# Kernel tuning notes

Measured on AMD Instinct MI355X. Metric: run time of the kernel, lower is better.

Reference implementation:

```python
import jax, jax.numpy as jnp
import numpy as np

B, T, H, HEADS, OUT = 16, 8192, 256, 2, 5
PERIOD = 16  # phoneme boundary every 16 frames
EPS_DENOM = 1e-5
LN_EPS = 1e-5
TEMP = 1.0


def setup_inputs() -> dict:
    key = jax.random.key(0)
    ks = jax.random.split(key, 8)
    s = 0.02
    feat = jax.random.normal(ks[0], (B, T, H), jnp.float32)
    ph_bd = jnp.broadcast_to(((jnp.arange(T) % PERIOD) == PERIOD - 1).astype(jnp.int32), (B, T))
    ph_length = T // PERIOD + 1  # 513
    return {
        'feat': feat,
        'ph_bd': ph_bd,
        'ph_length': ph_length,
        'w_attn': jax.random.normal(ks[1], (HEADS, H), jnp.float32) * s,
        'b_attn': jnp.zeros((HEADS,), jnp.float32),
        'ln1_g': jnp.ones((H,), jnp.float32),
        'ln1_b': jnp.zeros((H,), jnp.float32),
        'conv1_w': jax.random.normal(ks[2], (H, H, 3), jnp.float32) * s,
        'conv1_b': jnp.zeros((H,), jnp.float32),
        'conv2_w': jax.random.normal(ks[3], (H, H, 1), jnp.float32) * s,
        'conv2_b': jnp.zeros((H,), jnp.float32),
        'ln2_g': jnp.ones((H,), jnp.float32),
        'ln2_b': jnp.zeros((H,), jnp.float32),
        'post_w': jax.random.normal(ks[4], (H, H, 3), jnp.float32) * s,
        'post_b': jnp.zeros((H,), jnp.float32),
        'w_out': jax.random.normal(ks[5], (OUT, H), jnp.float32) * s,
        'b_out': jnp.zeros((OUT,), jnp.float32),
    }


def _ln_c(x, g, b):
    # LayerNorm over channel dim of [B, C, L]
    m = jnp.mean(x, axis=1, keepdims=True)
    v = jnp.mean((x - m) ** 2, axis=1, keepdims=True)
    return (x - m) * jax.lax.rsqrt(v + LN_EPS) * g[None, :, None] + b[None, :, None]


def _conv1d(x, w, b):
    # x: [B, C, L], w: [O, I, K], 'same' padding
    pad = (w.shape[-1] - 1) // 2
    y = jax.lax.conv_general_dilated(x, w, (1,), [(pad, pad)],
                                     dimension_numbers=('NCH', 'OIH', 'NCH'))
    return y + b[None, :, None]


def reference(feat, ph_bd, ph_length, w_attn, b_attn, ln1_g, ln1_b,
              conv1_w, conv1_b, conv2_w, conv2_b, ln2_g, ln2_b,
              post_w, post_b, w_out, b_out):
    # multihead attention weights per frame: [B, T, heads]
    attn = jax.nn.sigmoid(jnp.einsum('bth,ah->bta', feat, w_attn) + b_attn)
    attn_mean = jnp.mean(attn, axis=-1)                 # [B, T]
    # mean over heads of feat[...,None]*attn == feat * mean(attn)
    attn_feat = feat * attn_mean[..., None]             # [B, T, H]

    mel2ph = jnp.cumsum(ph_bd, axis=1)                  # [B, T] frame->phoneme id
    bidx = jnp.arange(feat.shape[0])[:, None]
    denom = jnp.zeros((feat.shape[0], ph_length), feat.dtype).at[bidx, mel2ph].add(attn_mean)
    ph_agg = jnp.zeros((feat.shape[0], ph_length, feat.shape[2]), feat.dtype).at[bidx, mel2ph].add(attn_feat)
    ph_agg = ph_agg / (denom[..., None] + EPS_DENOM)    # [B, L, H]

    # ConvBlocks (1 residual block, layers_in_block=1, c_multiple=1, swish)
    x = jnp.transpose(ph_agg, (0, 2, 1))                # [B, H, L]
    nonpad = (jnp.sum(jnp.abs(x), axis=1) > 0).astype(x.dtype)[:, None, :]
    h = _ln_c(x, ln1_g, ln1_b)
    h = _conv1d(h, conv1_w, conv1_b) * (3.0 ** -0.5)
    h = jax.nn.silu(h)
    h = _conv1d(h, conv2_w, conv2_b)
    x = (x + h) * nonpad
    x = _ln_c(x, ln2_g, ln2_b) * nonpad
    x = _conv1d(x, post_w, post_b) * nonpad
    out = jnp.transpose(x, (0, 2, 1))                   # [B, L, H]

    tech_logits = (jnp.einsum('blh,oh->blo', out, w_out) + b_out) / TEMP
    return tech_logits
```

## Files before the change

### kernel.cpp

```cpp
#include <hip/hip_runtime.h>
#include <hip/hip_bf16.h>

#define TDIM 8192
#define BDIM 16
#define HDIM 256
#define PHL  513
#define PADL 515
#define MROWS (BDIM*PHL)
#define SEGW 514

typedef __attribute__((ext_vector_type(8))) short  short8;
typedef __attribute__((ext_vector_type(4))) float  floatx4;

__device__ __forceinline__ float sigmoidf_(float x){ return 1.0f/(1.0f+__expf(-x)); }

typedef __attribute__((address_space(1))) const unsigned int gu32;
typedef __attribute__((address_space(3))) unsigned int lu32;
__device__ __forceinline__ void g2l16(const void* g, void* l){
  __builtin_amdgcn_global_load_lds((gu32*)g, (lu32*)l, 16, 0, 0);
}

__device__ __forceinline__ float blk_reduce(float v, float* red){
  #pragma unroll
  for (int off=32; off>0; off>>=1) v += __shfl_xor(v, off, 64);
  int w = threadIdx.x>>6;
  __syncthreads();
  if ((threadIdx.x&63)==0) red[w]=v;
  __syncthreads();
  return red[0]+red[1]+red[2]+red[3];
}

__global__ __launch_bounds__(256) void k_scan(const int* __restrict__ ph_bd,
                                              int* __restrict__ seg){
  int b = blockIdx.x, tid = threadIdx.x;
  const int* in = ph_bd + (size_t)b*TDIM;
  int sb = b*SEGW;
  int base = tid*32;
  int vals[32]; int s=0;
  #pragma unroll
  for (int i=0;i<32;i+=4){
    int4 v = *(const int4*)(in+base+i);
    vals[i]=v.x; vals[i+1]=v.y; vals[i+2]=v.z; vals[i+3]=v.w;
    s += v.x+v.y+v.z+v.w;
  }
  __shared__ int ls[256];
  ls[tid]=s; __syncthreads();
  for (int off=1; off<256; off<<=1){
    int t = (tid>=off)? ls[tid-off] : 0;
    __syncthreads();
    ls[tid]+=t;
    __syncthreads();
  }
  int cur = ls[tid]-s;
  #pragma unroll
  for (int i=0;i<32;i++){
    int nxt = cur + vals[i];
    for (int v=cur+1; v<=nxt; v++) seg[sb+v] = base+i;
    cur = nxt;
  }
  if (tid==0) seg[sb] = 0;
  if (tid==255){ for (int v=cur+1; v<SEGW; v++) seg[sb+v] = TDIM; }
}

__global__ __launch_bounds__(256) void k_prep(
    const float* __restrict__ conv1_w, const float* __restrict__ conv2_w,
    const float* __restrict__ post_w,
    __bf16* __restrict__ w1t, __bf16* __restrict__ w2t, __bf16* __restrict__ w3t,
    int* __restrict__ rowoff,
    float* __restrict__ x0pad, __bf16* __restrict__ h1pad, __bf16* __restrict__ x2pad)
{
  int idx = blockIdx.x*256 + threadIdx.x;
  if (idx < 256*768){
    int o = idx/768, j = idx - o*768;
    int dl = j>>8, i = j&255;
    int src = (o*256+i)*3 + dl;
    w1t[idx] = (__bf16)conv1_w[src];
    w3t[idx] = (__bf16)post_w[src];
  }
  if (idx < 256*256)
    w2t[idx] = (__bf16)conv2_w[idx];
  if (idx < MROWS){
    int b = idx/513, l = idx - b*513;
    rowoff[idx] = (b*PADL + l)*HDIM;
  }
  if (idx < BDIM*2*HDIM){
    int b = idx>>9, rr=(idx>>8)&1, c=idx&255;
    size_t row = (size_t)b*PADL + (rr? (PADL-1):0);
    x0pad[row*HDIM+c]=0.f;
    h1pad[row*HDIM+c]=(__bf16)0.f;
    x2pad[row*HDIM+c]=(__bf16)0.f;
  }
}

__global__ __launch_bounds__(256) void k_attn(
    const float* __restrict__ feat, const int* __restrict__ seg,
    const float* __restrict__ w_attn, const float* __restrict__ b_attn,
    const float* __restrict__ ln1_g, const float* __restrict__ ln1_b,
    float* __restrict__ x0pad, __bf16* __restrict__ h1pad, float* __restrict__ nonpad)
{
  int b = blockIdx.x / PHL, p = blockIdx.x - b*PHL;
  int tid = threadIdx.x, lane = tid&63, w = tid>>6;
  __shared__ float4 sfeat[16*64];
  __shared__ float sam[16];
  __shared__ float red[4];

  int t0 = seg[b*SEGW + p], t1 = seg[b*SEGW + p + 1];

  float4 wa0 = ((const float4*)w_attn)[lane];
  float4 wa1 = ((const float4*)(w_attn+HDIM))[lane];
  float ba0 = b_attn[0], ba1 = b_attn[1];

  float agg=0.f, denom=0.f;
  for (int base=t0; base<t1; base+=16){
    int nf = min(16, t1-base);
    const float4* src = (const float4*)(feat + ((size_t)b*TDIM + base)*HDIM);
    for (int idx=tid; idx<nf*64; idx+=256) sfeat[idx] = src[idx];
    __syncthreads();
    for (int ft=w; ft<nf; ft+=4){
      float4 f = sfeat[ft*64+lane];
      float d0 = f.x*wa0.x + f.y*wa0.y + f.z*wa0.z + f.w*wa0.w;
      float d1 = f.x*wa1.x + f.y*wa1.y + f.z*wa1.z + f.w*wa1.w;
      #pragma unroll
      for (int off=32;off>0;off>>=1){ d0+=__shfl_xor(d0,off,64); d1+=__shfl_xor(d1,off,64); }
      if (lane==0) sam[ft] = 0.5f*(sigmoidf_(d0+ba0)+sigmoidf_(d1+ba1));
    }
    __syncthreads();
    const float* sf = (const float*)sfeat;
    for (int ft=0; ft<nf; ft++){ float a=sam[ft]; agg += sf[ft*HDIM+tid]*a; denom += a; }
    __syncthreads();
  }

  float x = agg/(denom+1e-5f);
  float sabs = blk_reduce(fabsf(x), red);
  float np = (sabs>0.f)?1.f:0.f;
  float mean = blk_reduce(x, red)*(1.f/HDIM);
  float d = x-mean;
  float var = blk_reduce(d*d, red)*(1.f/HDIM);
  float h = d*rsqrtf(var+1e-5f)*ln1_g[tid]+ln1_b[tid];

  size_t off = ((size_t)b*PADL + p + 1)*HDIM;
  x0pad[off+tid]=x;
  h1pad[off+tid]=(__bf16)h;
  if (tid==0) nonpad[blockIdx.x]=np;
}

__global__ __launch_bounds__(256) void k_convblock(
    const short* __restrict__ h1pad, const int* __restrict__ rowoff,
    const short* __restrict__ w1t, const short* __restrict__ w2t,
    const float* __restrict__ c1b, const float* __restrict__ c2b,
    const float* __restrict__ x0pad, const float* __restrict__ nonpad,
    const float* __restrict__ g2, const float* __restrict__ b2,
    __bf16* __restrict__ x2pad)
{
  __shared__ __align__(16) short As[4*64*8];
  __shared__ __align__(16) short Bs[4*256*8];
  __shared__ __align__(16) short Gt[32*64*8];
  int tid=threadIdx.x, lane=tid&63, w=tid>>6, quad=lane>>4, l15=lane&15;
  int m0 = blockIdx.x*64;
  int am = min(m0 + lane, MROWS-1);
  const short* aRow = h1pad + rowoff[am];
  short* AsW = &As[w*64*8];

  floatx4 acc[16];
  #pragma unroll
  for (int i=0;i<16;i++) acc[i] = (floatx4){0.f,0.f,0.f,0.f};

  for (int chunk=0; chunk<24; chunk++){
    int k0 = chunk*32;
    g2l16(aRow + k0 + w*8, AsW);
    #pragma unroll
    for (int ng=0; ng<4; ng++)
      g2l16(w1t + (size_t)(ng*64+lane)*768 + k0 + w*8, &Bs[(w*256 + ng*64)*8]);
    __syncthreads();
    short8 af = *(const short8*)&As[(quad*64 + w*16 + l15)*8];
    #pragma unroll
    for (int nt=0; nt<16; nt++){
      short8 bf = *(const short8*)&Bs[(quad*256 + nt*16 + l15)*8];
      acc[nt] = __builtin_amdgcn_mfma_f32_16x16x32_bf16(af, bf, acc[nt], 0,0,0);
    }
    __syncthreads();
  }

  const float inv_s3 = 0.57735026918962576f;
  #pragma unroll
  for (int nt=0; nt<16; nt++){
    int n = nt*16 + l15;
    float bias = c1b[n];
    #pragma unroll
    for (int r=0;r<4;r++){
      float v = (acc[nt][r] + bias)*inv_s3;
      v = v*sigmoidf_(v);
      int ml = w*16 + quad*4 + r;
      ((__bf16*)Gt)[((n>>3)*64 + ml)*8 + (n&7)] = (__bf16)v;
    }
  }

  floatx4 acc2[16];
  #pragma unroll
  for (int i=0;i<16;i++) acc2[i] = (floatx4){0.f,0.f,0.f,0.f};
  for (int chunk=0; chunk<8; chunk++){
    int k0 = chunk*32;
    #pragma unroll
    for (int ng=0; ng<4; ng++)
      g2l16(w2t + (size_t)(ng*64+lane)*256 + k0 + w*8, &Bs[(w*256 + ng*64)*8]);
    __syncthreads();
    short8 af = *(const short8*)&Gt[((chunk*4+quad)*64 + w*16 + l15)*8];
    #pragma unroll
    for (int nt=0; nt<16; nt++){
      short8 bf = *(const short8*)&Bs[(quad*256 + nt*16 + l15)*8];
      acc2[nt] = __builtin_amdgcn_mfma_f32_16x16x32_bf16(af, bf, acc2[nt], 0,0,0);
    }
    __syncthreads();
  }

  int mbase = m0 + w*16 + quad*4;
  float np_[4]; const float* x0b[4]; int roff[4];
  #pragma unroll
  for (int r=0;r<4;r++){
    int m = min(mbase + r, MROWS-1);
    np_[r] = nonpad[m];
    roff[r] = rowoff[m] + HDIM;
    x0b[r] = x0pad + roff[r];
  }
  float sum[4]={0,0,0,0}, ssq[4]={0,0,0,0};
  #pragma unroll
  for (int nt=0; nt<16; nt++){
    int n = nt*16 + l15;
    float cb = c2b[n];
    #pragma unroll
    for (int r=0;r<4;r++){
      float x = (x0b[r][n] + acc2[nt][r] + cb)*np_[r];
      acc2[nt][r] = x;
      sum[r]+=x; ssq[r]+=x*x;
    }
  }
  #pragma unroll
  for (int off=1; off<16; off<<=1){
    #pragma unroll
    for (int r=0;r<4;r++){ sum[r]+=__shfl_xor(sum[r],off,64); ssq[r]+=__shfl_xor(ssq[r],off,64); }
  }
  float mean[4], rs[4];
  #pragma unroll
  for (int r=0;r<4;r++){
    mean[r]=sum[r]*(1.f/HDIM);
    float var=ssq[r]*(1.f/HDIM)-mean[r]*mean[r];
    rs[r]=rsqrtf(var+1e-5f);
  }
  #pragma unroll
  for (int nt=0; nt<16; nt++){
    int n = nt*16 + l15;
    float gg=g2[n], bb=b2[n];
    #pragma unroll
    for (int r=0;r<4;r++){
      int m = mbase + r;
      if (m < MROWS){
        float y = ((acc2[nt][r]-mean[r])*rs[r]*gg + bb)*np_[r];
        x2pad[roff[r]+n] = (__bf16)y;
      }
    }
  }
}

__global__ __launch_bounds__(256) void k_post(
    const short* __restrict__ x2pad, const int* __restrict__ rowoff,
    const short* __restrict__ w3t, const float* __restrict__ postb,
    const float* __restrict__ nonpad, const float* __restrict__ w_out,
    const float* __restrict__ b_out, float* __restrict__ dst)
{
  __shared__ __align__(16) short As[4*64*8];
  __shared__ __align__(16) short Bs[4*256*8];
  __shared__ float ws[5*256];
  int tid=threadIdx.x, lane=tid&63, w=tid>>6, quad=lane>>4, l15=lane&15;
  int m0 = blockIdx.x*64;
  int am = min(m0 + lane, MROWS-1);
  const short* aRow = x2pad + rowoff[am];
  short* AsW = &As[w*64*8];
  for (int i=tid; i<5*256; i+=256) ws[i]=w_out[i];

  floatx4 acc[16];
  #pragma unroll
  for (int i=0;i<16;i++) acc[i] = (floatx4){0.f,0.f,0.f,0.f};
  for (int chunk=0; chunk<24; chunk++){
    int k0 = chunk*32;
    g2l16(aRow + k0 + w*8, AsW);
    #pragma unroll
    for (int ng=0; ng<4; ng++)
      g2l16(w3t + (size_t)(ng*64+lane)*768 + k0 + w*8, &Bs[(w*256 + ng*64)*8]);
    __syncthreads();
    short8 af = *(const short8*)&As[(quad*64 + w*16 + l15)*8];
    #pragma unroll
    for (int nt=0; nt<16; nt++){
      short8 bf = *(const short8*)&Bs[(quad*256 + nt*16 + l15)*8];
      acc[nt] = __builtin_amdgcn_mfma_f32_16x16x32_bf16(af, bf, acc[nt], 0,0,0);
    }
    __syncthreads();
  }

  int mbase = m0 + w*16 + quad*4;
  float np_[4];
  #pragma unroll
  for (int r=0;r<4;r++) np_[r] = nonpad[min(mbase+r, MROWS-1)];
  float p[4][5];
  #pragma unroll
  for (int r=0;r<4;r++)
    #pragma unroll
    for (int o=0;o<5;o++) p[r][o]=0.f;
  #pragma unroll
  for (int nt=0; nt<16; nt++){
    int n = nt*16 + l15;
    float pb = postb[n];
    float wv[5];
    #pragma unroll
    for (int o=0;o<5;o++) wv[o]=ws[o*256+n];
    #pragma unroll
    for (int r=0;r<4;r++){
      float v = (acc[nt][r] + pb)*np_[r];
      #pragma unroll
      for (int o=0;o<5;o++) p[r][o] += v*wv[o];
    }
  }
  #pragma unroll
  for (int off=1; off<16; off<<=1)
    #pragma unroll
    for (int r=0;r<4;r++)
      #pragma unroll
      for (int o=0;o<5;o++) p[r][o]+=__shfl_xor(p[r][o],off,64);
  if (l15==0){
    #pragma unroll
    for (int r=0;r<4;r++){
      int m = mbase + r;
      if (m < MROWS){
        #pragma unroll
        for (int o=0;o<5;o++) dst[(size_t)m*5+o] = p[r][o] + b_out[o];
      }
    }
  }
}

extern "C" void kernel_launch(void* const* d_in, const int* in_sizes, int n_in,
                              void* d_out, int out_size, void* d_ws, size_t ws_size,
                              hipStream_t stream) {
  const float* feat    = (const float*)d_in[0];
  const int*   ph_bd   = (const int*)  d_in[1];
  const float* w_attn  = (const float*)d_in[3];
  const float* b_attn  = (const float*)d_in[4];
  const float* ln1_g   = (const float*)d_in[5];
  const float* ln1_b   = (const float*)d_in[6];
  const float* conv1_w = (const float*)d_in[7];
  const float* conv1_b = (const float*)d_in[8];
  const float* conv2_w = (const float*)d_in[9];
  const float* conv2_b = (const float*)d_in[10];
  const float* ln2_g   = (const float*)d_in[11];
  const float* ln2_b   = (const float*)d_in[12];
  const float* post_w  = (const float*)d_in[13];
  const float* post_b  = (const float*)d_in[14];
  const float* w_out   = (const float*)d_in[15];
  const float* b_out   = (const float*)d_in[16];

  char* wp = (char*)d_ws;
  auto alloc = [&](size_t bytes)->void*{
    void* p = (void*)wp; wp += (bytes + 255) & ~(size_t)255; return p;
  };
  int*    seg    = (int*)   alloc((size_t)BDIM*SEGW*4);
  int*    rowoff = (int*)   alloc((size_t)MROWS*4);
  float*  x0pad  = (float*) alloc((size_t)BDIM*PADL*HDIM*4);
  __bf16* h1pad  = (__bf16*)alloc((size_t)BDIM*PADL*HDIM*2);
  __bf16* x2pad  = (__bf16*)alloc((size_t)BDIM*PADL*HDIM*2);
  float*  nonpad = (float*) alloc((size_t)MROWS*4);
  __bf16* w1t    = (__bf16*)alloc((size_t)256*768*2);
  __bf16* w2t    = (__bf16*)alloc((size_t)256*256*2);
  __bf16* w3t    = (__bf16*)alloc((size_t)256*768*2);

  k_scan<<<BDIM, 256, 0, stream>>>(ph_bd, seg);
  k_prep<<<768, 256, 0, stream>>>(conv1_w, conv2_w, post_w, w1t, w2t, w3t,
                                  rowoff, x0pad, h1pad, x2pad);
  k_attn<<<MROWS, 256, 0, stream>>>(feat, seg, w_attn, b_attn,
                                    ln1_g, ln1_b, x0pad, h1pad, nonpad);
  k_convblock<<<129, 256, 0, stream>>>((const short*)h1pad, rowoff, (const short*)w1t,
                                       (const short*)w2t, conv1_b, conv2_b,
                                       x0pad, nonpad, ln2_g, ln2_b, x2pad);
  k_post<<<129, 256, 0, stream>>>((const short*)x2pad, rowoff, (const short*)w3t,
                                  post_b, nonpad, w_out, b_out, (float*)d_out);
}
```

Measured before the change: 309.7 us.

## Halve GEMM row tile to 32, split N across warp pairs, merge scan and prep

New measurement: 301.8 us. 1.03x faster.

```diff
diff --git a/kernel.cpp b/kernel.cpp
--- a/kernel.cpp
+++ b/kernel.cpp
@@ -30,46 +30,47 @@
   return red[0]+red[1]+red[2]+red[3];
 }
 
-__global__ __launch_bounds__(256) void k_scan(const int* __restrict__ ph_bd,
-                                              int* __restrict__ seg){
-  int b = blockIdx.x, tid = threadIdx.x;
-  const int* in = ph_bd + (size_t)b*TDIM;
-  int sb = b*SEGW;
-  int base = tid*32;
-  int vals[32]; int s=0;
-  #pragma unroll
-  for (int i=0;i<32;i+=4){
-    int4 v = *(const int4*)(in+base+i);
-    vals[i]=v.x; vals[i+1]=v.y; vals[i+2]=v.z; vals[i+3]=v.w;
-    s += v.x+v.y+v.z+v.w;
-  }
-  __shared__ int ls[256];
-  ls[tid]=s; __syncthreads();
-  for (int off=1; off<256; off<<=1){
-    int t = (tid>=off)? ls[tid-off] : 0;
-    __syncthreads();
-    ls[tid]+=t;
-    __syncthreads();
-  }
-  int cur = ls[tid]-s;
-  #pragma unroll
-  for (int i=0;i<32;i++){
-    int nxt = cur + vals[i];
-    for (int v=cur+1; v<=nxt; v++) seg[sb+v] = base+i;
-    cur = nxt;
-  }
-  if (tid==0) seg[sb] = 0;
-  if (tid==255){ for (int v=cur+1; v<SEGW; v++) seg[sb+v] = TDIM; }
-}
-
-__global__ __launch_bounds__(256) void k_prep(
+__global__ __launch_bounds__(256) void k_init(
+    const int* __restrict__ ph_bd, int* __restrict__ seg,
     const float* __restrict__ conv1_w, const float* __restrict__ conv2_w,
     const float* __restrict__ post_w,
     __bf16* __restrict__ w1t, __bf16* __restrict__ w2t, __bf16* __restrict__ w3t,
     int* __restrict__ rowoff,
     float* __restrict__ x0pad, __bf16* __restrict__ h1pad, __bf16* __restrict__ x2pad)
 {
-  int idx = blockIdx.x*256 + threadIdx.x;
+  int tid = threadIdx.x;
+  if (blockIdx.x < BDIM){
+    int b = blockIdx.x;
+    const int* in = ph_bd + (size_t)b*TDIM;
+    int sb = b*SEGW;
+    int base = tid*32;
+    int vals[32]; int s=0;
+    #pragma unroll
+    for (int i=0;i<32;i+=4){
+      int4 v = *(const int4*)(in+base+i);
+      vals[i]=v.x; vals[i+1]=v.y; vals[i+2]=v.z; vals[i+3]=v.w;
+      s += v.x+v.y+v.z+v.w;
+    }
+    __shared__ int ls[256];
+    ls[tid]=s; __syncthreads();
+    for (int off=1; off<256; off<<=1){
+      int t = (tid>=off)? ls[tid-off] : 0;
+      __syncthreads();
+      ls[tid]+=t;
+      __syncthreads();
+    }
+    int cur = ls[tid]-s;
+    #pragma unroll
+    for (int i=0;i<32;i++){
+      int nxt = cur + vals[i];
+      for (int v=cur+1; v<=nxt; v++) seg[sb+v] = base+i;
+      cur = nxt;
+    }
+    if (tid==0) seg[sb] = 0;
+    if (tid==255){ for (int v=cur+1; v<SEGW; v++) seg[sb+v] = TDIM; }
+    return;
+  }
+  int idx = (blockIdx.x-BDIM)*256 + tid;
   if (idx < 256*768){
     int o = idx/768, j = idx - o*768;
     int dl = j>>8, i = j&255;
@@ -152,30 +153,31 @@
     const float* __restrict__ g2, const float* __restrict__ b2,
     __bf16* __restrict__ x2pad)
 {
-  __shared__ __align__(16) short As[4*64*8];
+  __shared__ __align__(16) short As[4*32*8];
   __shared__ __align__(16) short Bs[4*256*8];
-  __shared__ __align__(16) short Gt[32*64*8];
+  __shared__ __align__(16) short Gt[32*32*8];
+  __shared__ float s_sum[4][16], s_ssq[4][16];
   int tid=threadIdx.x, lane=tid&63, w=tid>>6, quad=lane>>4, l15=lane&15;
-  int m0 = blockIdx.x*64;
-  int am = min(m0 + lane, MROWS-1);
-  const short* aRow = h1pad + rowoff[am];
-  short* AsW = &As[w*64*8];
-
-  floatx4 acc[16];
-  #pragma unroll
-  for (int i=0;i<16;i++) acc[i] = (floatx4){0.f,0.f,0.f,0.f};
+  int g = w>>1, n0w = (w&1)*128;
+  int m0 = blockIdx.x*32;
+  int arow = min(m0 + (lane&31), MROWS-1);
+  const short* aPtr = h1pad + rowoff[arow] + (2*w + (lane>>5))*8;
+
+  floatx4 acc[8];
+  #pragma unroll
+  for (int i=0;i<8;i++) acc[i] = (floatx4){0.f,0.f,0.f,0.f};
 
   for (int chunk=0; chunk<24; chunk++){
     int k0 = chunk*32;
-    g2l16(aRow + k0 + w*8, AsW);
+    if (w < 2) g2l16(aPtr + k0, &As[w*64*8]);
     #pragma unroll
     for (int ng=0; ng<4; ng++)
       g2l16(w1t + (size_t)(ng*64+lane)*768 + k0 + w*8, &Bs[(w*256 + ng*64)*8]);
     __syncthreads();
-    short8 af = *(const short8*)&As[(quad*64 + w*16 + l15)*8];
-    #pragma unroll
-    for (int nt=0; nt<16; nt++){
-      short8 bf = *(const short8*)&Bs[(quad*256 + nt*16 + l15)*8];
+    short8 af = *(const short8*)&As[(quad*32 + g*16 + l15)*8];
+    #pragma unroll
+    for (int nt=0; nt<8; nt++){
+      short8 bf = *(const short8*)&Bs[(quad*256 + n0w + nt*16 + l15)*8];
       acc[nt] = __builtin_amdgcn_mfma_f32_16x16x32_bf16(af, bf, acc[nt], 0,0,0);
     }
     __syncthreads();
@@ -183,53 +185,52 @@
 
   const float inv_s3 = 0.57735026918962576f;
   #pragma unroll
-  for (int nt=0; nt<16; nt++){
-    int n = nt*16 + l15;
+  for (int nt=0; nt<8; nt++){
+    int n = n0w + nt*16 + l15;
     float bias = c1b[n];
     #pragma unroll
     for (int r=0;r<4;r++){
       float v = (acc[nt][r] + bias)*inv_s3;
       v = v*sigmoidf_(v);
-      int ml = w*16 + quad*4 + r;
-      ((__bf16*)Gt)[((n>>3)*64 + ml)*8 + (n&7)] = (__bf16)v;
-    }
-  }
-
-  floatx4 acc2[16];
-  #pragma unroll
-  for (int i=0;i<16;i++) acc2[i] = (floatx4){0.f,0.f,0.f,0.f};
+      int m = g*16 + quad*4 + r;
+      ((__bf16*)Gt)[((n>>3)*32 + m)*8 + (n&7)] = (__bf16)v;
+    }
+  }
+
+  floatx4 acc2[8];
+  #pragma unroll
+  for (int i=0;i<8;i++) acc2[i] = (floatx4){0.f,0.f,0.f,0.f};
   for (int chunk=0; chunk<8; chunk++){
     int k0 = chunk*32;
     #pragma unroll
     for (int ng=0; ng<4; ng++)
       g2l16(w2t + (size_t)(ng*64+lane)*256 + k0 + w*8, &Bs[(w*256 + ng*64)*8]);
     __syncthreads();
-    short8 af = *(const short8*)&Gt[((chunk*4+quad)*64 + w*16 + l15)*8];
-    #pragma unroll
-    for (int nt=0; nt<16; nt++){
-      short8 bf = *(const short8*)&Bs[(quad*256 + nt*16 + l15)*8];
+    short8 af = *(const short8*)&Gt[((chunk*4+quad)*32 + g*16 + l15)*8];
+    #pragma unroll
+    for (int nt=0; nt<8; nt++){
+      short8 bf = *(const short8*)&Bs[(quad*256 + n0w + nt*16 + l15)*8];
       acc2[nt] = __builtin_amdgcn_mfma_f32_16x16x32_bf16(af, bf, acc2[nt], 0,0,0);
     }
     __syncthreads();
   }
 
-  int mbase = m0 + w*16 + quad*4;
-  float np_[4]; const float* x0b[4]; int roff[4];
+  int mbase = m0 + g*16 + quad*4;
+  float np_[4]; int roff[4];
   #pragma unroll
   for (int r=0;r<4;r++){
-    int m = min(mbase + r, MROWS-1);
-    np_[r] = nonpad[m];
-    roff[r] = rowoff[m] + HDIM;
-    x0b[r] = x0pad + roff[r];
+    int mm = min(mbase + r, MROWS-1);
+    np_[r] = nonpad[mm];
+    roff[r] = rowoff[mm] + HDIM;
   }
   float sum[4]={0,0,0,0}, ssq[4]={0,0,0,0};
   #pragma unroll
-  for (int nt=0; nt<16; nt++){
-    int n = nt*16 + l15;
+  for (int nt=0; nt<8; nt++){
+    int n = n0w + nt*16 + l15;
     float cb = c2b[n];
     #pragma unroll
     for (int r=0;r<4;r++){
-      float x = (x0b[r][n] + acc2[nt][r] + cb)*np_[r];
+      float x = (x0pad[roff[r]+n] + acc2[nt][r] + cb)*np_[r];
       acc2[nt][r] = x;
       sum[r]+=x; ssq[r]+=x*x;
     }
@@ -239,21 +240,28 @@
     #pragma unroll
     for (int r=0;r<4;r++){ sum[r]+=__shfl_xor(sum[r],off,64); ssq[r]+=__shfl_xor(ssq[r],off,64); }
   }
+  if (l15==0){
+    #pragma unroll
+    for (int r=0;r<4;r++){ s_sum[w][quad*4+r]=sum[r]; s_ssq[w][quad*4+r]=ssq[r]; }
+  }
+  __syncthreads();
   float mean[4], rs[4];
   #pragma unroll
   for (int r=0;r<4;r++){
-    mean[r]=sum[r]*(1.f/HDIM);
-    float var=ssq[r]*(1.f/HDIM)-mean[r]*mean[r];
-    rs[r]=rsqrtf(var+1e-5f);
-  }
-  #pragma unroll
-  for (int nt=0; nt<16; nt++){
-    int n = nt*16 + l15;
+    int i = quad*4+r;
+    float ts = s_sum[w&~1][i] + s_sum[w|1][i];
+    float tq = s_ssq[w&~1][i] + s_ssq[w|1][i];
+    mean[r] = ts*(1.f/HDIM);
+    float var = tq*(1.f/HDIM) - mean[r]*mean[r];
+    rs[r] = rsqrtf(var+1e-5f);
+  }
+  #pragma unroll
+  for (int nt=0; nt<8; nt++){
+    int n = n0w + nt*16 + l15;
     float gg=g2[n], bb=b2[n];
     #pragma unroll
     for (int r=0;r<4;r++){
-      int m = mbase + r;
-      if (m < MROWS){
+      if (mbase + r < MROWS){
         float y = ((acc2[nt][r]-mean[r])*rs[r]*gg + bb)*np_[r];
         x2pad[roff[r]+n] = (__bf16)y;
       }
@@ -267,36 +275,37 @@
     const float* __restrict__ nonpad, const float* __restrict__ w_out,
     const float* __restrict__ b_out, float* __restrict__ dst)
 {
-  __shared__ __align__(16) short As[4*64*8];
+  __shared__ __align__(16) short As[4*32*8];
   __shared__ __align__(16) short Bs[4*256*8];
   __shared__ float ws[5*256];
+  __shared__ float s_log[4][16][5];
   int tid=threadIdx.x, lane=tid&63, w=tid>>6, quad=lane>>4, l15=lane&15;
-  int m0 = blockIdx.x*64;
-  int am = min(m0 + lane, MROWS-1);
-  const short* aRow = x2pad + rowoff[am];
-  short* AsW = &As[w*64*8];
+  int g = w>>1, n0w = (w&1)*128;
+  int m0 = blockIdx.x*32;
+  int arow = min(m0 + (lane&31), MROWS-1);
+  const short* aPtr = x2pad + rowoff[arow] + (2*w + (lane>>5))*8;
   for (int i=tid; i<5*256; i+=256) ws[i]=w_out[i];
 
-  floatx4 acc[16];
-  #pragma unroll
-  for (int i=0;i<16;i++) acc[i] = (floatx4){0.f,0.f,0.f,0.f};
+  floatx4 acc[8];
+  #pragma unroll
+  for (int i=0;i<8;i++) acc[i] = (floatx4){0.f,0.f,0.f,0.f};
   for (int chunk=0; chunk<24; chunk++){
     int k0 = chunk*32;
-    g2l16(aRow + k0 + w*8, AsW);
+    if (w < 2) g2l16(aPtr + k0, &As[w*64*8]);
     #pragma unroll
     for (int ng=0; ng<4; ng++)
       g2l16(w3t + (size_t)(ng*64+lane)*768 + k0 + w*8, &Bs[(w*256 + ng*64)*8]);
     __syncthreads();
-    short8 af = *(const short8*)&As[(quad*64 + w*16 + l15)*8];
-    #pragma unroll
-    for (int nt=0; nt<16; nt++){
-      short8 bf = *(const short8*)&Bs[(quad*256 + nt*16 + l15)*8];
+    short8 af = *(const short8*)&As[(quad*32 + g*16 + l15)*8];
+    #pragma unroll
+    for (int nt=0; nt<8; nt++){
+      short8 bf = *(const short8*)&Bs[(quad*256 + n0w + nt*16 + l15)*8];
       acc[nt] = __builtin_amdgcn_mfma_f32_16x16x32_bf16(af, bf, acc[nt], 0,0,0);
     }
     __syncthreads();
   }
 
-  int mbase = m0 + w*16 + quad*4;
+  int mbase = m0 + g*16 + quad*4;
   float np_[4];
   #pragma unroll
   for (int r=0;r<4;r++) np_[r] = nonpad[min(mbase+r, MROWS-1)];
@@ -306,8 +315,8 @@
     #pragma unroll
     for (int o=0;o<5;o++) p[r][o]=0.f;
   #pragma unroll
-  for (int nt=0; nt<16; nt++){
-    int n = nt*16 + l15;
+  for (int nt=0; nt<8; nt++){
+    int n = n0w + nt*16 + l15;
     float pb = postb[n];
     float wv[5];
     #pragma unroll
@@ -327,11 +336,20 @@
       for (int o=0;o<5;o++) p[r][o]+=__shfl_xor(p[r][o],off,64);
   if (l15==0){
     #pragma unroll
+    for (int r=0;r<4;r++)
+      #pragma unroll
+      for (int o=0;o<5;o++) s_log[w][quad*4+r][o]=p[r][o];
+  }
+  __syncthreads();
+  if (l15==0 && (w&1)==0){
+    #pragma unroll
     for (int r=0;r<4;r++){
       int m = mbase + r;
       if (m < MROWS){
+        int i = quad*4+r;
         #pragma unroll
-        for (int o=0;o<5;o++) dst[(size_t)m*5+o] = p[r][o] + b_out[o];
+        for (int o=0;o<5;o++)
+          dst[(size_t)m*5+o] = s_log[w][i][o] + s_log[w+1][i][o] + b_out[o];
       }
     }
   }
@@ -371,14 +389,13 @@
   __bf16* w2t    = (__bf16*)alloc((size_t)256*256*2);
   __bf16* w3t    = (__bf16*)alloc((size_t)256*768*2);
 
-  k_scan<<<BDIM, 256, 0, stream>>>(ph_bd, seg);
-  k_prep<<<768, 256, 0, stream>>>(conv1_w, conv2_w, post_w, w1t, w2t, w3t,
-                                  rowoff, x0pad, h1pad, x2pad);
+  k_init<<<BDIM+768, 256, 0, stream>>>(ph_bd, seg, conv1_w, conv2_w, post_w,
+                                       w1t, w2t, w3t, rowoff, x0pad, h1pad, x2pad);
   k_attn<<<MROWS, 256, 0, stream>>>(feat, seg, w_attn, b_attn,
                                     ln1_g, ln1_b, x0pad, h1pad, nonpad);
-  k_convblock<<<129, 256, 0, stream>>>((const short*)h1pad, rowoff, (const short*)w1t,
+  k_convblock<<<257, 256, 0, stream>>>((const short*)h1pad, rowoff, (const short*)w1t,
                                        (const short*)w2t, conv1_b, conv2_b,
                                        x0pad, nonpad, ln2_g, ln2_b, x2pad);
-  k_post<<<129, 256, 0, stream>>>((const short*)x2pad, rowoff, (const short*)w3t,
+  k_post<<<257, 256, 0, stream>>>((const short*)x2pad, rowoff, (const short*)w3t,
                                   post_b, nonpad, w_out, b_out, (float*)d_out);
 }
```
